# Kernel optimization log

Hardware: AMD Instinct MI355X
Metric: run time of the kernel (lower is better)

The kernel has to match this reference:

```python
import jax, jax.numpy as jnp
from jax import lax
import numpy as np

H = 1024   # num_hidden
B = 256    # batch_size
T = 256    # seq_length
C = 10     # num_classes


def setup_inputs() -> dict:
    key = jax.random.key(0)
    ks = jax.random.split(key, 10)
    def xav(k, shape):
        fan_in, fan_out = shape[1], shape[0]
        std = jnp.sqrt(2.0 / (fan_in + fan_out))
        return jax.random.normal(k, shape, dtype=jnp.float32) * std
    return {
        "x": jax.random.normal(ks[0], (B, T), dtype=jnp.float32),
        "W_gx": xav(ks[1], (H, 1)), "W_gh": xav(ks[2], (H, H)),
        "W_ix": xav(ks[3], (H, 1)), "W_ih": xav(ks[4], (H, H)),
        "W_fx": xav(ks[5], (H, 1)), "W_fh": xav(ks[6], (H, H)),
        "W_ox": xav(ks[7], (H, 1)), "W_oh": xav(ks[8], (H, H)),
        "W_ph": xav(ks[9], (C, H)),
        "b_g": jnp.zeros((H, 1), jnp.float32),
        "b_i": jnp.zeros((H, 1), jnp.float32),
        "b_f": jnp.zeros((H, 1), jnp.float32),
        "b_o": jnp.zeros((H, 1), jnp.float32),
        "b_p": jnp.zeros((C, 1), jnp.float32),
    }


def reference(x, W_gx, W_gh, W_ix, W_ih, W_fx, W_fh, W_ox, W_oh, W_ph,
              b_g, b_i, b_f, b_o, b_p):
    # x: [B, T]; per-step input is a (1, B) row, states h,c are [H, B].
    xs = jnp.swapaxes(x, 0, 1)[:, None, :]  # [T, 1, B]

    def step(carry, x_t):
        h, c = carry
        g = jnp.tanh(W_gx @ x_t + W_gh @ h + b_g)
        i = jax.nn.sigmoid(W_ix @ x_t + W_ih @ h + b_i)
        f = jax.nn.sigmoid(W_fx @ x_t + W_fh @ h + b_f)
        o = jax.nn.sigmoid(W_ox @ x_t + W_oh @ h + b_o)
        c = g * i + c * f
        h = jnp.tanh(c) * o
        return (h, c), None

    h0 = jnp.zeros((W_gh.shape[0], x.shape[0]), x.dtype)
    (h, c), _ = lax.scan(step, (h0, h0), xs)
    return (W_ph @ h + b_p).T  # [B, C]
```

## Files before the change

kernel.cpp:

```cpp
#include <hip/hip_runtime.h>
#include <hip/hip_fp16.h>

#define H_ 1024
#define B_ 256
#define T_ 256
#define C_ 10

typedef _Float16 f16x8 __attribute__((ext_vector_type(8)));
typedef float f32x4 __attribute__((ext_vector_type(4)));

__device__ __forceinline__ float sigm_f(float v) { return 1.f / (1.f + __expf(-v)); }
__device__ __forceinline__ float tanh_f(float v) {
  v = fminf(fmaxf(v, -15.f), 15.f);
  float e = __expf(2.f * v);
  return (e - 1.f) / (e + 1.f);
}

__device__ __forceinline__ f16x8 load_h8_agent(const _Float16* p) {
  const unsigned long long* q = reinterpret_cast<const unsigned long long*>(p);
  unsigned long long lo = __hip_atomic_load(q,     __ATOMIC_RELAXED, __HIP_MEMORY_SCOPE_AGENT);
  unsigned long long hi = __hip_atomic_load(q + 1, __ATOMIC_RELAXED, __HIP_MEMORY_SCOPE_AGENT);
  union { unsigned long long u[2]; f16x8 v; } r;
  r.u[0] = lo; r.u[1] = hi;
  return r.v;
}

__global__ void lstm_init(unsigned* __restrict__ flags, int flagDw,
                          unsigned* __restrict__ scal,
                          unsigned* __restrict__ h0u, int h0Dw) {
  int i = blockIdx.x * blockDim.x + threadIdx.x;
  int n = gridDim.x * blockDim.x;
  for (int k = i; k < flagDw; k += n)
    __hip_atomic_store(flags + k, 0u, __ATOMIC_RELAXED, __HIP_MEMORY_SCOPE_AGENT);
  for (int k = i; k < 1024; k += n)
    __hip_atomic_store(scal + k, 0u, __ATOMIC_RELAXED, __HIP_MEMORY_SCOPE_AGENT);
  for (int k = i; k < h0Dw; k += n)
    __hip_atomic_store(h0u + k, 0u, __ATOMIC_RELAXED, __HIP_MEMORY_SCOPE_AGENT);
}

__global__ __launch_bounds__(512, 2) void lstm_main(
    const float* __restrict__ x,
    const float* __restrict__ Wgh, const float* __restrict__ Wih,
    const float* __restrict__ Wfh, const float* __restrict__ Woh,
    const float* __restrict__ Wgx, const float* __restrict__ Wix,
    const float* __restrict__ Wfx, const float* __restrict__ Wox,
    const float* __restrict__ bg, const float* __restrict__ bi,
    const float* __restrict__ bf, const float* __restrict__ bo,
    _Float16* __restrict__ hT, unsigned int* __restrict__ flags,
    unsigned int* __restrict__ scal, int rot)
{
  const int bid  = blockIdx.x;
  const int g    = bid & 7;
  const int r    = bid >> 3;
  const int tid  = threadIdx.x;
  const int wid  = tid >> 6;
  const int lane = tid & 63;
  const int mg   = wid >> 2;
  const int kg   = wid & 3;
  const int q    = lane >> 4;
  const int rlo  = lane & 15;
  const int c0   = g * 32;
  const size_t HB = (size_t)B_ * H_;

  __shared__ float part[32 * 4 * 128];
  __shared__ unsigned mode_sh;

  {
    unsigned xcc;
    asm volatile("s_getreg_b32 %0, hwreg(HW_REG_XCC_ID)" : "=s"(xcc));
    if (tid == 0) {
      unsigned* mask  = scal + g;
      unsigned* ready = scal + 8 + g;
      __hip_atomic_fetch_or(mask, 1u << (xcc & 31),
                            __ATOMIC_RELAXED, __HIP_MEMORY_SCOPE_AGENT);
      __hip_atomic_fetch_add(ready, 1u, __ATOMIC_RELEASE, __HIP_MEMORY_SCOPE_AGENT);
      int gd = 0; bool trip = false;
      while (__hip_atomic_load(ready, __ATOMIC_RELAXED, __HIP_MEMORY_SCOPE_AGENT) < 32u) {
        if (++gd > (1 << 22)) { trip = true; break; }
        __builtin_amdgcn_s_sleep(8);
      }
      unsigned m = __hip_atomic_load(mask, __ATOMIC_ACQUIRE, __HIP_MEMORY_SCOPE_AGENT);
      mode_sh = (rot && !trip && __popc((int)m) == 1) ? 1u : 2u;
    }
    __syncthreads();
  }
  const bool fast = (mode_sh == 1u);

  f16x8 A[32];
  {
    const int gate = rlo & 3;
    const float* Wsel = (gate == 0) ? Wgh : (gate == 1) ? Wih : (gate == 2) ? Wfh : Woh;
    #pragma unroll
    for (int f = 0; f < 32; ++f) {
      const int mt  = f >> 3, kkl = f & 7;
      const int u   = mg * 16 + mt * 4 + (rlo >> 2);
      const int k   = kg * 256 + kkl * 32 + q * 8;
      const float4* p = reinterpret_cast<const float4*>(
          Wsel + (size_t)(r * 32 + u) * H_ + k);
      float4 lo = p[0], hi = p[1];
      f16x8 a;
      a[0]=(_Float16)lo.x; a[1]=(_Float16)lo.y; a[2]=(_Float16)lo.z; a[3]=(_Float16)lo.w;
      a[4]=(_Float16)hi.x; a[5]=(_Float16)hi.y; a[6]=(_Float16)hi.z; a[7]=(_Float16)hi.w;
      A[f] = a;
    }
  }

  const int c_l = tid >> 4;
  const int uu  = tid & 15;
  float wx0[4], wx1[4], bb0[4], bb1[4];
  {
    const int u0 = r * 32 + uu, u1 = u0 + 16;
    wx0[0]=Wgx[u0]; wx0[1]=Wix[u0]; wx0[2]=Wfx[u0]; wx0[3]=Wox[u0];
    wx1[0]=Wgx[u1]; wx1[1]=Wix[u1]; wx1[2]=Wfx[u1]; wx1[3]=Wox[u1];
    bb0[0]=bg[u0];  bb0[1]=bi[u0];  bb0[2]=bf[u0];  bb0[3]=bo[u0];
    bb1[0]=bg[u1];  bb1[1]=bi[u1];  bb1[2]=bf[u1];  bb1[3]=bo[u1];
  }
  float cs0 = 0.f, cs1 = 0.f;
  const float* xrow = x + (size_t)(c0 + c_l) * T_;

  const int flagIdxPoll = (g * 32 + kg * 8 + (lane & 7)) * 16;
  const int flagIdxOwn  = (g * 32 + r) * 16;

  for (int t = 0; t < T_; ++t) {
    const _Float16* hbr = hT + (size_t)(rot ? t : (t & 1)) * HB;
    _Float16*       hbw = hT + (size_t)(rot ? (t + 1) : ((t + 1) & 1)) * HB;
    unsigned* pub  = (rot ? flags + (size_t)t * 4096 : flags) + flagIdxOwn;

    if (t > 0) {
      unsigned* myf = (rot ? flags + (size_t)(t - 1) * 4096 : flags) + flagIdxPoll;
      const unsigned tgt = rot ? 1u : (unsigned)t;
      int guard = 0;
      for (;;) {
        unsigned v = tgt;
        if (lane < 8)
          v = __hip_atomic_load(myf, __ATOMIC_RELAXED, __HIP_MEMORY_SCOPE_AGENT);
        if (__all((int)(v >= tgt))) break;
        if (++guard > (1 << 19)) break;
        __builtin_amdgcn_s_sleep(1);
      }
      asm volatile("" ::: "memory");
    }

    const _Float16* hb0 = hbr + (size_t)(c0 + rlo) * H_ + kg * 256 + q * 8;
    const _Float16* hb1 = hb0 + 16 * (size_t)H_;

    f16x8 B0[8], B1[8];
    if (fast) {
      #pragma unroll
      for (int kkl = 0; kkl < 8; ++kkl) {
        B0[kkl] = *reinterpret_cast<const f16x8*>(hb0 + kkl * 32);
        B1[kkl] = *reinterpret_cast<const f16x8*>(hb1 + kkl * 32);
      }
    } else {
      #pragma unroll
      for (int kkl = 0; kkl < 8; ++kkl) {
        B0[kkl] = load_h8_agent(hb0 + kkl * 32);
        B1[kkl] = load_h8_agent(hb1 + kkl * 32);
      }
    }

    f32x4 acc[4][2];
    #pragma unroll
    for (int mt = 0; mt < 4; ++mt) {
      acc[mt][0] = (f32x4){0.f, 0.f, 0.f, 0.f};
      acc[mt][1] = (f32x4){0.f, 0.f, 0.f, 0.f};
    }
    #pragma unroll
    for (int kkl = 0; kkl < 8; ++kkl) {
      #pragma unroll
      for (int mt = 0; mt < 4; ++mt) {
        acc[mt][0] = __builtin_amdgcn_mfma_f32_16x16x32_f16(A[mt*8+kkl], B0[kkl], acc[mt][0], 0, 0, 0);
        acc[mt][1] = __builtin_amdgcn_mfma_f32_16x16x32_f16(A[mt*8+kkl], B1[kkl], acc[mt][1], 0, 0, 0);
      }
    }

    #pragma unroll
    for (int mt = 0; mt < 4; ++mt) {
      #pragma unroll
      for (int nt = 0; nt < 2; ++nt) {
        const int c_loc = nt * 16 + rlo;
        const int m = mg * 64 + mt * 16 + 4 * q;
        unsigned addr = (unsigned)(c_loc * 2048 + kg * 512 + m * 4);
        addr ^= (unsigned)((c_loc & 7) << 4);
        *reinterpret_cast<f32x4*>(reinterpret_cast<char*>(part) + addr) = acc[mt][nt];
      }
    }
    __syncthreads();

    const float xv = xrow[t];
    unsigned short hbits0, hbits1;
    {
      unsigned lin = (unsigned)(c_l * 2048 + uu * 16);
      f32x4 s = *reinterpret_cast<const f32x4*>(
          reinterpret_cast<const char*>(part) + (lin ^ ((unsigned)(c_l & 7) << 4)));
      #pragma unroll
      for (int kgi = 1; kgi < 4; ++kgi) {
        unsigned l2 = lin + (unsigned)(kgi * 512);
        s += *reinterpret_cast<const f32x4*>(
            reinterpret_cast<const char*>(part) + (l2 ^ ((unsigned)(c_l & 7) << 4)));
      }
      float pg = s[0] + wx0[0]*xv + bb0[0];
      float pi = s[1] + wx0[1]*xv + bb0[1];
      float pf = s[2] + wx0[2]*xv + bb0[2];
      float po = s[3] + wx0[3]*xv + bb0[3];
      float gg = tanh_f(pg), ii = sigm_f(pi), ff = sigm_f(pf), oo = sigm_f(po);
      cs0 = gg * ii + cs0 * ff;
      hbits0 = __builtin_bit_cast(unsigned short, (_Float16)(tanh_f(cs0) * oo));
    }
    {
      unsigned lin = (unsigned)(c_l * 2048 + (uu + 16) * 16);
      f32x4 s = *reinterpret_cast<const f32x4*>(
          reinterpret_cast<const char*>(part) + (lin ^ ((unsigned)(c_l & 7) << 4)));
      #pragma unroll
      for (int kgi = 1; kgi < 4; ++kgi) {
        unsigned l2 = lin + (unsigned)(kgi * 512);
        s += *reinterpret_cast<const f32x4*>(
            reinterpret_cast<const char*>(part) + (l2 ^ ((unsigned)(c_l & 7) << 4)));
      }
      float pg = s[0] + wx1[0]*xv + bb1[0];
      float pi = s[1] + wx1[1]*xv + bb1[1];
      float pf = s[2] + wx1[2]*xv + bb1[2];
      float po = s[3] + wx1[3]*xv + bb1[3];
      float gg = tanh_f(pg), ii = sigm_f(pi), ff = sigm_f(pf), oo = sigm_f(po);
      cs1 = gg * ii + cs1 * ff;
      hbits1 = __builtin_bit_cast(unsigned short, (_Float16)(tanh_f(cs1) * oo));
    }

    {
      _Float16* hout = hbw + (size_t)(c0 + c_l) * H_ + r * 32;
      int nb0 = __shfl_down((int)hbits0, 1);
      int nb1 = __shfl_down((int)hbits1, 1);
      if ((uu & 1) == 0) {
        unsigned v0 = (unsigned)hbits0 | ((unsigned)(unsigned short)nb0 << 16);
        unsigned v1 = (unsigned)hbits1 | ((unsigned)(unsigned short)nb1 << 16);
        unsigned int* p0 = reinterpret_cast<unsigned int*>(hout + uu);
        unsigned int* p1 = reinterpret_cast<unsigned int*>(hout + uu + 16);
        if (fast && t != T_ - 1) {
          *(volatile unsigned int*)p0 = v0;
          *(volatile unsigned int*)p1 = v1;
        } else {
          __hip_atomic_store(p0, v0, __ATOMIC_RELAXED, __HIP_MEMORY_SCOPE_AGENT);
          __hip_atomic_store(p1, v1, __ATOMIC_RELAXED, __HIP_MEMORY_SCOPE_AGENT);
        }
      }
    }
    asm volatile("s_waitcnt vmcnt(0)" ::: "memory");
    __syncthreads();
    if (tid == 0)
      __hip_atomic_store(pub, rot ? 1u : (unsigned)(t + 1),
                         __ATOMIC_RELAXED, __HIP_MEMORY_SCOPE_AGENT);
  }
}

__global__ void lstm_proj(const _Float16* __restrict__ hfin,
                          const float* __restrict__ Wph,
                          const float* __restrict__ bp,
                          float* __restrict__ out)
{
  const int b = blockIdx.x;
  const int l = threadIdx.x;
  const _Float16* hrow = hfin + (size_t)b * H_;
  float p[C_];
  #pragma unroll
  for (int cls = 0; cls < C_; ++cls) p[cls] = 0.f;
  for (int u = l; u < H_; u += 64) {
    float hv = (float)hrow[u];
    #pragma unroll
    for (int cls = 0; cls < C_; ++cls) p[cls] += hv * Wph[cls * H_ + u];
  }
  #pragma unroll
  for (int cls = 0; cls < C_; ++cls) {
    float v = p[cls];
    #pragma unroll
    for (int off = 32; off > 0; off >>= 1) v += __shfl_down(v, off);
    if (l == 0) out[b * C_ + cls] = v + bp[cls];
  }
}

extern "C" void kernel_launch(void* const* d_in, const int* in_sizes, int n_in,
                              void* d_out, int out_size, void* d_ws, size_t ws_size,
                              hipStream_t stream) {
  const float* x   = (const float*)d_in[0];
  const float* Wgx = (const float*)d_in[1];
  const float* Wgh = (const float*)d_in[2];
  const float* Wix = (const float*)d_in[3];
  const float* Wih = (const float*)d_in[4];
  const float* Wfx = (const float*)d_in[5];
  const float* Wfh = (const float*)d_in[6];
  const float* Wox = (const float*)d_in[7];
  const float* Woh = (const float*)d_in[8];
  const float* Wph = (const float*)d_in[9];
  const float* bg  = (const float*)d_in[10];
  const float* bi  = (const float*)d_in[11];
  const float* bf  = (const float*)d_in[12];
  const float* bo  = (const float*)d_in[13];
  const float* bp  = (const float*)d_in[14];
  float* out = (float*)d_out;

  const size_t HB = (size_t)B_ * H_;
  const size_t need = (8u << 20) + (size_t)(T_ + 1) * HB * sizeof(_Float16);
  const int rot = (ws_size >= need) ? 1 : 0;

  unsigned *flags, *scal; _Float16 *hT; int flagDw;
  if (rot) {
    flags  = (unsigned*)d_ws;
    scal   = (unsigned*)((char*)d_ws + (4u << 20));
    hT     = (_Float16*)((char*)d_ws + (8u << 20));
    flagDw = T_ * 4096;
  } else {
    hT     = (_Float16*)d_ws;
    flags  = (unsigned*)((char*)d_ws + 2 * HB * sizeof(_Float16));
    scal   = flags + 4096;
    flagDw = 4096;
  }

  lstm_init<<<256, 256, 0, stream>>>(flags, flagDw, scal,
                                     (unsigned*)hT, (int)(HB / 2));
  lstm_main<<<256, 512, 0, stream>>>(x, Wgh, Wih, Wfh, Woh,
                                     Wgx, Wix, Wfx, Wox,
                                     bg, bi, bf, bo, hT, flags, scal, rot);
  lstm_proj<<<256, 64, 0, stream>>>(hT + (size_t)(rot ? T_ : 0) * HB,
                                    Wph, bp, out);
}
```

Measured before the change: 1.712 ms.

## Replace per-step rotating hidden buffers with double buffer plus L1 invalidate

Removes the T+1 rotating hidden-state buffers and per-timestep flag arrays. It always uses a two-slot ping-pong buffer with monotonically increasing step counters as flags. In fast mode, where all blocks of a group share one XCC, it issues buffer_inv sc0 after the poll, so plain cached loads still see fresh h values. This cuts workspace size and init cost, keeps hidden state hot in cache, and lets fast mode run without the large workspace. The poll guard limits also change. The risk is stale reads if the L1 invalidate is not enough for coherence.

```diff
diff --git a/kernel.cpp b/kernel.cpp
--- a/kernel.cpp
+++ b/kernel.cpp
@@ -14,6 +14,10 @@
   v = fminf(fmaxf(v, -15.f), 15.f);
   float e = __expf(2.f * v);
   return (e - 1.f) / (e + 1.f);
+}
+
+__device__ __forceinline__ void inv_l1_wait() {
+  asm volatile("buffer_inv sc0\n\ts_waitcnt vmcnt(0)" ::: "memory");
 }
 
 __device__ __forceinline__ f16x8 load_h8_agent(const _Float16* p) {
@@ -47,7 +51,7 @@
     const float* __restrict__ bg, const float* __restrict__ bi,
     const float* __restrict__ bf, const float* __restrict__ bo,
     _Float16* __restrict__ hT, unsigned int* __restrict__ flags,
-    unsigned int* __restrict__ scal, int rot)
+    unsigned int* __restrict__ scal)
 {
   const int bid  = blockIdx.x;
   const int g    = bid & 7;
@@ -80,7 +84,7 @@
         __builtin_amdgcn_s_sleep(8);
       }
       unsigned m = __hip_atomic_load(mask, __ATOMIC_ACQUIRE, __HIP_MEMORY_SCOPE_AGENT);
-      mode_sh = (rot && !trip && __popc((int)m) == 1) ? 1u : 2u;
+      mode_sh = (!trip && __popc((int)m) == 1) ? 1u : 2u;
     }
     __syncthreads();
   }
@@ -118,28 +122,28 @@
   float cs0 = 0.f, cs1 = 0.f;
   const float* xrow = x + (size_t)(c0 + c_l) * T_;
 
-  const int flagIdxPoll = (g * 32 + kg * 8 + (lane & 7)) * 16;
-  const int flagIdxOwn  = (g * 32 + r) * 16;
+  unsigned int* myflags = flags + ((size_t)(g * 32 + kg * 8 + (lane & 7)) * 16);
+  unsigned int* ownflag = flags + ((size_t)(g * 32 + r) * 16);
 
   for (int t = 0; t < T_; ++t) {
-    const _Float16* hbr = hT + (size_t)(rot ? t : (t & 1)) * HB;
-    _Float16*       hbw = hT + (size_t)(rot ? (t + 1) : ((t + 1) & 1)) * HB;
-    unsigned* pub  = (rot ? flags + (size_t)t * 4096 : flags) + flagIdxOwn;
-
     if (t > 0) {
-      unsigned* myf = (rot ? flags + (size_t)(t - 1) * 4096 : flags) + flagIdxPoll;
-      const unsigned tgt = rot ? 1u : (unsigned)t;
+      const unsigned tgt = (unsigned)t;
       int guard = 0;
+      const int gmax = fast ? (1 << 18) : (1 << 20);
       for (;;) {
         unsigned v = tgt;
         if (lane < 8)
-          v = __hip_atomic_load(myf, __ATOMIC_RELAXED, __HIP_MEMORY_SCOPE_AGENT);
+          v = __hip_atomic_load(myflags, __ATOMIC_RELAXED, __HIP_MEMORY_SCOPE_AGENT);
         if (__all((int)(v >= tgt))) break;
-        if (++guard > (1 << 19)) break;
+        if (++guard > gmax) break;
         __builtin_amdgcn_s_sleep(1);
       }
       asm volatile("" ::: "memory");
-    }
+      if (fast) inv_l1_wait();
+    }
+
+    const _Float16* hbr = hT + (size_t)(t & 1) * HB;
+    _Float16*       hbw = hT + (size_t)((t + 1) & 1) * HB;
 
     const _Float16* hb0 = hbr + (size_t)(c0 + rlo) * H_ + kg * 256 + q * 8;
     const _Float16* hb1 = hb0 + 16 * (size_t)H_;
@@ -247,7 +251,7 @@
     asm volatile("s_waitcnt vmcnt(0)" ::: "memory");
     __syncthreads();
     if (tid == 0)
-      __hip_atomic_store(pub, rot ? 1u : (unsigned)(t + 1),
+      __hip_atomic_store(ownflag, (unsigned)(t + 1),
                          __ATOMIC_RELAXED, __HIP_MEMORY_SCOPE_AGENT);
   }
 }
@@ -297,28 +301,15 @@
   const float* bp  = (const float*)d_in[14];
   float* out = (float*)d_out;
 
-  const size_t HB = (size_t)B_ * H_;
-  const size_t need = (8u << 20) + (size_t)(T_ + 1) * HB * sizeof(_Float16);
-  const int rot = (ws_size >= need) ? 1 : 0;
-
-  unsigned *flags, *scal; _Float16 *hT; int flagDw;
-  if (rot) {
-    flags  = (unsigned*)d_ws;
-    scal   = (unsigned*)((char*)d_ws + (4u << 20));
-    hT     = (_Float16*)((char*)d_ws + (8u << 20));
-    flagDw = T_ * 4096;
-  } else {
-    hT     = (_Float16*)d_ws;
-    flags  = (unsigned*)((char*)d_ws + 2 * HB * sizeof(_Float16));
-    scal   = flags + 4096;
-    flagDw = 4096;
-  }
-
-  lstm_init<<<256, 256, 0, stream>>>(flags, flagDw, scal,
-                                     (unsigned*)hT, (int)(HB / 2));
+  _Float16* hT = (_Float16*)d_ws;
+  const size_t hT_bytes = (size_t)2 * B_ * H_ * sizeof(_Float16);
+  unsigned int* flags = (unsigned int*)((char*)d_ws + hT_bytes);
+  unsigned int* scal  = (unsigned int*)((char*)d_ws + hT_bytes + 16384);
+
+  lstm_init<<<256, 256, 0, stream>>>(flags, 4096, scal,
+                                     (unsigned*)hT, (int)(B_ * H_ / 2));
   lstm_main<<<256, 512, 0, stream>>>(x, Wgh, Wih, Wfh, Woh,
                                      Wgx, Wix, Wfx, Wox,
-                                     bg, bi, bf, bo, hT, flags, scal, rot);
-  lstm_proj<<<256, 64, 0, stream>>>(hT + (size_t)(rot ? T_ : 0) * HB,
-                                    Wph, bp, out);
-}
+                                     bg, bi, bf, bo, hT, flags, scal);
+  lstm_proj<<<256, 64, 0, stream>>>(hT, Wph, bp, out);
+}
```

After: 1.793 ms. +4.8%, slower.
